# Optimization experiments

Hardware: AMD Instinct MI355X
Metric: run time of the kernel (lower is better)

The kernel has to match this reference:

```python
import jax, jax.numpy as jnp
import numpy as np

TAU = 1.0  # smooth-max temperature for the SW-score proxy


def setup_inputs() -> dict:
    key = jax.random.key(0)
    k1, k2 = jax.random.split(key)
    B, L, D, H = 24, 512, 64, 64
    x = jax.random.normal(k1, (B, L, D), dtype=jnp.float32)
    W = jax.random.normal(k2, (D, H), dtype=jnp.float32) * 0.1
    b = jnp.zeros((H,), dtype=jnp.float32)
    return {"x": x, "W": W, "b": b}


def reference(x, W, b):
    # Per-residue encoder (shared across all pair invocations in the original).
    h = jax.nn.gelu(x @ W + b)                      # [B, L, H]
    # All unique pairs in ONE batched contraction instead of O(B^2) tiny
    # 2-example model calls: substitution/similarity tensor for every pair.
    S = jnp.einsum('ilh,jmh->ijlm', h, h)           # [B, B, L, L]
    # Smooth Smith-Waterman score proxy: temperature-scaled soft-max over
    # all residue-pair scores -> one scalar per sequence pair.
    scores = TAU * jax.nn.logsumexp(S / TAU, axis=(2, 3))  # [B, B]
    # S is symmetric in (i, j), so scores[i, j] == scores[j, i], matching
    # the original's reuse of scores[j*batch + i] for i > j.
    return scores
```

## Files before the change

kernel.cpp:

```cpp
#include <hip/hip_runtime.h>
#include <hip/hip_bf16.h>


#define LOG2E 1.4426950408889634f

typedef unsigned short u16;
typedef __attribute__((ext_vector_type(8))) short bf16x8;
typedef __attribute__((ext_vector_type(4))) float f32x4;

static __device__ __forceinline__ u16 bf16bits(float f) {
  __hip_bfloat16 h = __float2bfloat16(f);
  return *reinterpret_cast<u16*>(&h);
}

static __device__ __forceinline__ float fast_exp2(float x) {
  int i = (int)fmaf(x, 8388608.0f, 1065098601.0f);
  return __int_as_float(i);
}

__global__ __launch_bounds__(256) void encode_kernel(
    const float* __restrict__ x, const float* __restrict__ W,
    const float* __restrict__ bias, u16* __restrict__ hb,
    u16* __restrict__ hlb) {
  int lane = threadIdx.x & 63;
  int wid = threadIdx.x >> 6;
  int row0 = (blockIdx.x * 4 + wid) * 16;
  int r = lane & 15;
  int kg = lane >> 4;

  bf16x8 xa[2];
#pragma unroll
  for (int kh = 0; kh < 2; ++kh) {
    const float* xp = x + (size_t)(row0 + r) * 64 + kh * 32 + kg * 8;
    bf16x8 v;
#pragma unroll
    for (int e = 0; e < 8; ++e) v[e] = (short)bf16bits(xp[e]);
    xa[kh] = v;
  }

  bf16x8 wf[4][2];
#pragma unroll
  for (int nb = 0; nb < 4; ++nb)
#pragma unroll
    for (int kh = 0; kh < 2; ++kh) {
      bf16x8 v;
#pragma unroll
      for (int e = 0; e < 8; ++e)
        v[e] = (short)bf16bits(W[(kh * 32 + kg * 8 + e) * 64 + nb * 16 + r]);
      wf[nb][kh] = v;
    }

  const f32x4 zero = {0.f, 0.f, 0.f, 0.f};
#pragma unroll
  for (int nb = 0; nb < 4; ++nb) {
    f32x4 acc = __builtin_amdgcn_mfma_f32_16x16x32_bf16(xa[0], wf[nb][0], zero, 0, 0, 0);
    acc = __builtin_amdgcn_mfma_f32_16x16x32_bf16(xa[1], wf[nb][1], acc, 0, 0, 0);
    float bb = bias[nb * 16 + r];
#pragma unroll
    for (int q = 0; q < 4; ++q) {
      float z = acc[q] + bb;
      float t = tanhf(0.7978845608028654f * (z + 0.044715f * z * z * z));
      float g = 0.5f * z * (1.0f + t);
      size_t o = (size_t)(row0 + kg * 4 + q) * 64 + nb * 16 + r;
      hb[o] = bf16bits(g);
      hlb[o] = bf16bits(g * LOG2E);
    }
  }
}

__global__ __launch_bounds__(256) void pair_kernel(
    const u16* __restrict__ hb, const u16* __restrict__ hlb,
    float* __restrict__ part) {
  __shared__ char smem[32768];

  int idx = blockIdx.x;
  int p = idx >> 2;
  int tile = idx & 3;
  int rh = tile >> 1;
  int ch = tile & 1;
  int i = 0, rem = p;
  while (rem >= 24 - i) { rem -= 24 - i; ++i; }
  int j = i + rem;

  const u16* Ap = hb + (size_t)i * 512 * 64;
  const char* Bbytes =
      (const char*)(hlb + (size_t)j * 512 * 64) + (size_t)ch * 256 * 128;

  int wid = threadIdx.x >> 6;
  int lane = threadIdx.x & 63;
  int r = lane & 15;
  int kg = lane >> 4;
  int row0 = rh * 256 + wid * 64;

  bf16x8 a[4][2];
#pragma unroll
  for (int rm = 0; rm < 4; ++rm)
#pragma unroll
    for (int kf = 0; kf < 2; ++kf)
      a[rm][kf] = *reinterpret_cast<const bf16x8*>(
          Ap + (size_t)(row0 + rm * 16 + r) * 64 + kf * 32 + kg * 8);

#pragma unroll
  for (int c = 0; c < 8; ++c) {
    int obase = (wid * 8 + c) * 1024;
    int o = obase + lane * 16;
    int src = o ^ (((o >> 7) & 7) << 4);
    __builtin_amdgcn_global_load_lds(
        (const __attribute__((address_space(1))) void*)(Bbytes + src),
        (__attribute__((address_space(3))) void*)(smem + obase), 16, 0, 0);
  }

  int sw = (r & 7) << 4;
  int off0 = r * 128 + ((kg * 16) ^ sw);
  int off1 = r * 128 + ((64 + kg * 16) ^ sw);

  __syncthreads();

  float s0 = 0.f, s1 = 0.f, s2 = 0.f, s3 = 0.f;
  const f32x4 zero = {0.f, 0.f, 0.f, 0.f};

#pragma unroll
  for (int cn = 0; cn < 16; ++cn) {
    const char* bp = smem + cn * 2048;
    bf16x8 b0 = *reinterpret_cast<const bf16x8*>(bp + off0);
    bf16x8 b1 = *reinterpret_cast<const bf16x8*>(bp + off1);
#pragma unroll
    for (int rm = 0; rm < 4; ++rm) {
      f32x4 acc = __builtin_amdgcn_mfma_f32_16x16x32_bf16(a[rm][0], b0, zero, 0, 0, 0);
      acc = __builtin_amdgcn_mfma_f32_16x16x32_bf16(a[rm][1], b1, acc, 0, 0, 0);
      s0 += fast_exp2(acc[0]);
      s1 += fast_exp2(acc[1]);
      s2 += fast_exp2(acc[2]);
      s3 += fast_exp2(acc[3]);
    }
  }
  float sum = (s0 + s1) + (s2 + s3);
#pragma unroll
  for (int off = 32; off >= 1; off >>= 1) sum += __shfl_xor(sum, off, 64);
  if (lane == 0) part[idx * 4 + wid] = sum;
}

__global__ void finish_kernel(const float* __restrict__ part,
                              float* __restrict__ out) {
  int t = threadIdx.x + blockIdx.x * blockDim.x;
  if (t >= 576) return;
  int i = t / 24, j = t % 24;
  int ii = i < j ? i : j, jj = i < j ? j : i;
  int p = ii * 24 - ii * (ii - 1) / 2 + (jj - ii);
  const f32x4* pv = reinterpret_cast<const f32x4*>(part + p * 16);
  float s = 0.f;
#pragma unroll
  for (int q = 0; q < 4; ++q) {
    f32x4 v = pv[q];
    s += (v[0] + v[1]) + (v[2] + v[3]);
  }
  out[t] = logf(s);
}

extern "C" void kernel_launch(void* const* d_in, const int* in_sizes, int n_in,
                              void* d_out, int out_size, void* d_ws,
                              size_t ws_size, hipStream_t stream) {
  const float* x = (const float*)d_in[0];
  const float* W = (const float*)d_in[1];
  const float* bias = (const float*)d_in[2];
  float* out = (float*)d_out;

  u16* hb = (u16*)d_ws;
  u16* hlb = hb + 12288 * 64;
  float* part = (float*)(hlb + 12288 * 64);

  encode_kernel<<<192, 256, 0, stream>>>(x, W, bias, hb, hlb);
  pair_kernel<<<1200, 256, 0, stream>>>(hb, hlb, part);
  finish_kernel<<<9, 64, 0, stream>>>(part, out);
}
```

Measured before the change: 27.89 us.

## Fuse final reduction into pair kernel via atomics and software-pipeline MFMA with exp

Removes the separate finish kernel: each pair block reduces its four wave sums in shared memory, atomically adds the result into a per-pair accumulator, and the last of the four tile blocks takes the log and writes both symmetric outputs. The encode kernel now runs as 768 one-wave blocks and also zeroes the accumulator and counter buffer. The pair loop is software-pipelined so the MFMAs for the next column chunk are issued before the exp2 accumulation of the current one. This trades a kernel launch for atomic traffic and a completion counter, and makes the summation order depend on which blocks finish first.

Result: slower. 45.89 us (+64.5%).

```diff
diff --git a/kernel.cpp b/kernel.cpp
--- a/kernel.cpp
+++ b/kernel.cpp
@@ -5,6 +5,7 @@
 #define LOG2E 1.4426950408889634f
 
 typedef unsigned short u16;
+typedef unsigned int u32;
 typedef __attribute__((ext_vector_type(8))) short bf16x8;
 typedef __attribute__((ext_vector_type(4))) float f32x4;
 
@@ -18,13 +19,17 @@
   return __int_as_float(i);
 }
 
-__global__ __launch_bounds__(256) void encode_kernel(
+__global__ __launch_bounds__(64) void encode_kernel(
     const float* __restrict__ x, const float* __restrict__ W,
     const float* __restrict__ bias, u16* __restrict__ hb,
-    u16* __restrict__ hlb) {
-  int lane = threadIdx.x & 63;
-  int wid = threadIdx.x >> 6;
-  int row0 = (blockIdx.x * 4 + wid) * 16;
+    u16* __restrict__ hlb, u32* __restrict__ sums_cnt) {
+  int lane = threadIdx.x;
+  if (blockIdx.x < 10) {
+    int t = blockIdx.x * 64 + lane;
+    if (t < 600) sums_cnt[t] = 0u;
+  }
+
+  int row0 = blockIdx.x * 16;
   int r = lane & 15;
   int kg = lane >> 4;
 
@@ -70,8 +75,11 @@
 
 __global__ __launch_bounds__(256) void pair_kernel(
     const u16* __restrict__ hb, const u16* __restrict__ hlb,
-    float* __restrict__ part) {
+    u32* __restrict__ sums_cnt, float* __restrict__ out) {
   __shared__ char smem[32768];
+
+  float* sums = (float*)sums_cnt;
+  u32* cnt = sums_cnt + 300;
 
   int idx = blockIdx.x;
   int p = idx >> 2;
@@ -116,45 +124,64 @@
 
   __syncthreads();
 
-  float s0 = 0.f, s1 = 0.f, s2 = 0.f, s3 = 0.f;
   const f32x4 zero = {0.f, 0.f, 0.f, 0.f};
-
-#pragma unroll
-  for (int cn = 0; cn < 16; ++cn) {
-    const char* bp = smem + cn * 2048;
-    bf16x8 b0 = *reinterpret_cast<const bf16x8*>(bp + off0);
-    bf16x8 b1 = *reinterpret_cast<const bf16x8*>(bp + off1);
+  f32x4 s[2] = {zero, zero};
+
+  f32x4 pA[4], pN[4];
+  {
+    bf16x8 b0 = *reinterpret_cast<const bf16x8*>(smem + off0);
+    bf16x8 b1 = *reinterpret_cast<const bf16x8*>(smem + off1);
 #pragma unroll
     for (int rm = 0; rm < 4; ++rm) {
-      f32x4 acc = __builtin_amdgcn_mfma_f32_16x16x32_bf16(a[rm][0], b0, zero, 0, 0, 0);
-      acc = __builtin_amdgcn_mfma_f32_16x16x32_bf16(a[rm][1], b1, acc, 0, 0, 0);
-      s0 += fast_exp2(acc[0]);
-      s1 += fast_exp2(acc[1]);
-      s2 += fast_exp2(acc[2]);
-      s3 += fast_exp2(acc[3]);
-    }
-  }
-  float sum = (s0 + s1) + (s2 + s3);
+      pA[rm] = __builtin_amdgcn_mfma_f32_16x16x32_bf16(a[rm][0], b0, zero, 0, 0, 0);
+      pA[rm] = __builtin_amdgcn_mfma_f32_16x16x32_bf16(a[rm][1], b1, pA[rm], 0, 0, 0);
+    }
+  }
+#pragma unroll
+  for (int cn = 1; cn <= 16; ++cn) {
+    if (cn < 16) {
+      const char* bp = smem + cn * 2048;
+      bf16x8 b0 = *reinterpret_cast<const bf16x8*>(bp + off0);
+      bf16x8 b1 = *reinterpret_cast<const bf16x8*>(bp + off1);
+#pragma unroll
+      for (int rm = 0; rm < 4; ++rm) {
+        pN[rm] = __builtin_amdgcn_mfma_f32_16x16x32_bf16(a[rm][0], b0, zero, 0, 0, 0);
+        pN[rm] = __builtin_amdgcn_mfma_f32_16x16x32_bf16(a[rm][1], b1, pN[rm], 0, 0, 0);
+      }
+    }
+#pragma unroll
+    for (int rm = 0; rm < 4; ++rm) {
+#pragma unroll
+      for (int q = 0; q < 4; ++q) s[rm & 1][q] += fast_exp2(pA[rm][q]);
+    }
+    if (cn < 16) {
+#pragma unroll
+      for (int rm = 0; rm < 4; ++rm) pA[rm] = pN[rm];
+    }
+  }
+
+  f32x4 sv = s[0] + s[1];
+  float sum = (sv[0] + sv[1]) + (sv[2] + sv[3]);
 #pragma unroll
   for (int off = 32; off >= 1; off >>= 1) sum += __shfl_xor(sum, off, 64);
-  if (lane == 0) part[idx * 4 + wid] = sum;
-}
-
-__global__ void finish_kernel(const float* __restrict__ part,
-                              float* __restrict__ out) {
-  int t = threadIdx.x + blockIdx.x * blockDim.x;
-  if (t >= 576) return;
-  int i = t / 24, j = t % 24;
-  int ii = i < j ? i : j, jj = i < j ? j : i;
-  int p = ii * 24 - ii * (ii - 1) / 2 + (jj - ii);
-  const f32x4* pv = reinterpret_cast<const f32x4*>(part + p * 16);
-  float s = 0.f;
-#pragma unroll
-  for (int q = 0; q < 4; ++q) {
-    f32x4 v = pv[q];
-    s += (v[0] + v[1]) + (v[2] + v[3]);
-  }
-  out[t] = logf(s);
+
+  __syncthreads();
+  if (lane == 0) *reinterpret_cast<float*>(smem + wid * 4) = sum;
+  __syncthreads();
+
+  if (threadIdx.x == 0) {
+    const float* sf = reinterpret_cast<const float*>(smem);
+    float bsum = (sf[0] + sf[1]) + (sf[2] + sf[3]);
+    atomicAdd(&sums[p], bsum);
+    __threadfence();
+    u32 n = atomicAdd(&cnt[p], 1u);
+    if (n == 3u) {
+      float total = atomicAdd(&sums[p], 0.0f);
+      float sc = logf(total);
+      out[i * 24 + j] = sc;
+      if (i != j) out[j * 24 + i] = sc;
+    }
+  }
 }
 
 extern "C" void kernel_launch(void* const* d_in, const int* in_sizes, int n_in,
@@ -167,9 +194,8 @@
 
   u16* hb = (u16*)d_ws;
   u16* hlb = hb + 12288 * 64;
-  float* part = (float*)(hlb + 12288 * 64);
-
-  encode_kernel<<<192, 256, 0, stream>>>(x, W, bias, hb, hlb);
-  pair_kernel<<<1200, 256, 0, stream>>>(hb, hlb, part);
-  finish_kernel<<<9, 64, 0, stream>>>(part, out);
-}
+  u32* sums_cnt = (u32*)(hlb + 12288 * 64);
+
+  encode_kernel<<<768, 64, 0, stream>>>(x, W, bias, hb, hlb, sums_cnt);
+  pair_kernel<<<1200, 256, 0, stream>>>(hb, hlb, sums_cnt, out);
+}
```
